# Kernel optimization log

Measured on AMD Instinct MI355X. Metric: run time of the kernel, lower is better.

## Reference

```python
import jax, jax.numpy as jnp
import numpy as np
from jax import lax

PATCH_SIZE = 7
NEIGH_SIZE = 9
SIGMA = 2.0
EPS = 1e-05


def _gaussian_kernel(sigma, sz):
    mid = sz // 2
    ax = np.arange(sz) - mid
    g = np.exp(-(ax[:, None] ** 2 + ax[None, :] ** 2) / (2.0 * sigma ** 2)) / (2.0 * np.pi * sigma ** 2)
    return g.astype(np.float32)


KERNEL = jnp.asarray(_gaussian_kernel(SIGMA, PATCH_SIZE))[None, None]  # (1,1,7,7)

_half = NEIGH_SIZE // 2
SHIFTS = jnp.asarray(
    [(x, y) for x in range(-_half, NEIGH_SIZE - _half)
     for y in range(-_half, NEIGH_SIZE - _half) if (x, y) != (0, 0)],
    dtype=jnp.int32)  # (80, 2) — xshift outer loop, yshift inner, matching torch order
SHIFTS4 = jnp.asarray([(-1, 0), (1, 0), (0, -1), (0, 1)], dtype=jnp.int32)


def _translate(img, tx, ty):
    # Faithful to torch affine_grid + grid_sample(nearest, zeros, align_corners=False):
    # a 'translation' of tx in normalized coords samples input at pixel j + tx*W/2.
    # H, W even and tx, ty integers -> exact integer pixel shifts, zero padding.
    H, W = img.shape
    px = jnp.arange(W) + tx * (W // 2)
    py = jnp.arange(H) + ty * (H // 2)
    mask = ((py >= 0) & (py < H))[:, None] & ((px >= 0) & (px < W))[None, :]
    out = img[jnp.clip(py, 0, H - 1)[:, None], jnp.clip(px, 0, W - 1)[None, :]]
    return jnp.where(mask, out, jnp.zeros((), img.dtype))


def _blur(x):
    # x: (N, H, W); conv2d with gaussian kernel, stride 1, padding 3 (same for 7x7)
    y = lax.conv_general_dilated(x[:, None], KERNEL, (1, 1), [(3, 3), (3, 3)],
                                 dimension_numbers=('NCHW', 'OIHW', 'NCHW'))
    return y[:, 0]


def _dp_batch(img2d, shifts):
    # Dp for a batch of shifts: shift, diff, square, gaussian blur
    shifted = jax.vmap(lambda s: _translate(img2d, s[0], s[1]))(shifts)  # (N,H,W)
    return _blur((img2d[None] - shifted) ** 2)


def setup_inputs() -> dict:
    key = jax.random.key(0)
    k1, k2 = jax.random.split(key)
    image1 = jax.random.normal(k1, (1, 1, 1024, 1024), dtype=jnp.float32)
    image2 = jax.random.normal(k2, (1, 1, 1024, 1024), dtype=jnp.float32)
    return {"image1": image1, "image2": image2}


def reference(image1, image2):
    img1 = image1[0, 0]  # (H, W)
    img2 = image2[0, 0]
    H, W = img1.shape
    reduce_size = (PATCH_SIZE + NEIGH_SIZE - 2) // 2  # = 7
    # Vimg: average of 4 single-pixel-neighborhood Dp's on image1, + eps
    Vimg = _dp_batch(img1, SHIFTS4).sum(axis=0) / 4.0 + EPS  # (H, W)
    # 80-shift MIND responses on image2
    D2 = _dp_batch(img2, SHIFTS)  # (80, H, W)
    mind = jnp.exp(-D2 / Vimg[None])
    # torch slices: dim1 end index is (C - reduce_size) = 1-7 = -6 -> H-6;
    # dim2 end index is (H - reduce_size). Replicated exactly (H == W).
    out = mind[:, reduce_size:H + 1 - reduce_size, reduce_size:H - reduce_size]
    mx = jnp.max(out, axis=0)
    return jnp.mean(out / mx[None])
```

## Files before the change

kernel.cpp:

```cpp
#include <hip/hip_runtime.h>
#include <cmath>

#define IMG_W 1024
#define TW 64
#define TH 16
#define PW 70
#define PH 22

struct GK { float gh[7]; float gv[7]; };

__global__ __launch_bounds__(256)
void mind_fused(const float* __restrict__ img1, const float* __restrict__ img2,
                float* __restrict__ out, GK gk)
{
    __shared__ float s1[4][PH][PW];
    __shared__ float s2[6][PH][TW];

    const int tx = (int)threadIdx.x;
    const int ty = (int)threadIdx.y;
    const int x0 = 7 + (int)blockIdx.x * TW;
    const int y0 = 7 + (int)blockIdx.y * TH;

    #pragma unroll
    for (int k = 0; k < 6; ++k) {
        const int r = 4 * k + ty;
        if (r < PH) {
            const int yy = min(y0 - 3 + r, 1023);
            const int yp = yy ^ 512;
            const float* __restrict__ r2  = img2 + yy * IMG_W;
            const float* __restrict__ r2p = img2 + yp * IMG_W;
            const float* __restrict__ r1  = img1 + yy * IMG_W;
            const float* __restrict__ r1p = img1 + yp * IMG_W;
            #pragma unroll
            for (int h = 0; h < 2; ++h) {
                const int c = tx + 64 * h;
                if (h == 0 || tx < PW - 64) {
                    const int xx = min(x0 - 3 + c, 1023);
                    const int xp = xx ^ 512;
                    const float a = r2[xx], b = r2[xp], cc = r2p[xx], d = r2p[xp];
                    const float a2 = a * a;
                    const float tb = a - b, tc = a - cc, td = a - d;
                    s1[0][r][c] = fmaf(tb, tb, -a2);
                    s1[1][r][c] = fmaf(tc, tc, -a2);
                    s1[2][r][c] = fmaf(td, td, -a2);
                    const float u = r1[xx], ub = r1[xp], uc = r1p[xx];
                    const float su = u - ub, sv = u - uc;
                    s1[3][r][c] = fmaf(u, u + u, fmaf(su, su, sv * sv));
                }
            }
        }
    }
    __syncthreads();

    #pragma unroll
    for (int k = 0; k < 6; ++k) {
        const int r = 4 * k + ty;
        if (r < PH) {
            float hlo = 0, hhi = 0, hv = 0, dlo = 0, dhi = 0, hu = 0;
            #pragma unroll
            for (int kx = 0; kx < 7; ++kx) {
                const float g = gk.gh[kx];
                const bool lo = (((x0 - 3 + tx + kx) & 512) == 0);
                const float gl  = lo ? g : 0.f;
                const float gh_ = lo ? 0.f : g;
                const float Hv = s1[0][r][tx + kx];
                const float Vv = s1[1][r][tx + kx];
                const float Dv = s1[2][r][tx + kx];
                const float Uv = s1[3][r][tx + kx];
                hlo = fmaf(gl,  Hv, hlo);
                hhi = fmaf(gh_, Hv, hhi);
                hv  = fmaf(g,   Vv, hv);
                dlo = fmaf(gl,  Dv, dlo);
                dhi = fmaf(gh_, Dv, dhi);
                hu  = fmaf(g,   Uv, hu);
            }
            s2[0][r][tx] = hlo; s2[1][r][tx] = hhi; s2[2][r][tx] = hv;
            s2[3][r][tx] = dlo; s2[4][r][tx] = dhi; s2[5][r][tx] = hu;
        }
    }
    __syncthreads();

    float f0[10], f1[10], f2[10], f3[10], f4[10], f5[10];
    #pragma unroll
    for (int r = 0; r < 10; ++r) {
        const int rr = 4 * ty + r;
        f0[r] = s2[0][rr][tx]; f1[r] = s2[1][rr][tx]; f2[r] = s2[2][rr][tx];
        f3[r] = s2[3][rr][tx]; f4[r] = s2[4][rr][tx]; f5[r] = s2[5][rr][tx];
    }

    const int xo = x0 + tx;
    float tsum = 0.f;
    #pragma unroll
    for (int k = 0; k < 4; ++k) {
        const int i  = 4 * ty + k;
        const int yo = y0 + i;
        float Ph = 0, Qh = 0, Pv = 0, Qv = 0, Ppp = 0, Pmp = 0, Ppm = 0, Pmm = 0, V4 = 0;
        #pragma unroll
        for (int ky = 0; ky < 7; ++ky) {
            const float g = gk.gv[ky];
            const bool ylo = (((yo - 3 + ky) & 512) == 0);
            const float wl = ylo ? g : 0.f;
            const float wh = ylo ? 0.f : g;
            const int idx = k + ky;
            Ph  = fmaf(g,  f0[idx], Ph);
            Qh  = fmaf(g,  f1[idx], Qh);
            Pv  = fmaf(wl, f2[idx], Pv);
            Qv  = fmaf(wh, f2[idx], Qv);
            Ppp = fmaf(wl, f3[idx], Ppp);
            Ppm = fmaf(wh, f3[idx], Ppm);
            Pmp = fmaf(wl, f4[idx], Pmp);
            Pmm = fmaf(wh, f4[idx], Pmm);
            V4  = fmaf(g,  f5[idx], V4);
        }
        const float V = fmaf(V4, 0.25f, 1e-5f);
        const float invV = 1.0f / V;
        float M = fminf(0.f, Ph);
        M = fminf(M, Qh);  M = fminf(M, Pv);  M = fminf(M, Qv);
        M = fminf(M, Ppp); M = fminf(M, Pmp); M = fminf(M, Ppm); M = fminf(M, Pmm);
        const float pix = 72.f * __expf(M * invV)
            + __expf((M - Ph ) * invV) + __expf((M - Qh ) * invV)
            + __expf((M - Pv ) * invV) + __expf((M - Qv ) * invV)
            + __expf((M - Ppp) * invV) + __expf((M - Pmp) * invV)
            + __expf((M - Ppm) * invV) + __expf((M - Pmm) * invV);
        const bool active = (xo <= 1016) && (yo <= 1017);
        tsum += active ? pix : 0.f;
    }

    #pragma unroll
    for (int off = 32; off > 0; off >>= 1)
        tsum += __shfl_down(tsum, off, 64);
    __shared__ float wsum[4];
    if (tx == 0) wsum[ty] = tsum;
    __syncthreads();
    if (tx == 0 && ty == 0) {
        const float bt = wsum[0] + wsum[1] + wsum[2] + wsum[3];
        atomicAdd(out, bt * (1.0f / 81688800.0f));
    }
}

extern "C" void kernel_launch(void* const* d_in, const int* in_sizes, int n_in,
                              void* d_out, int out_size, void* d_ws, size_t ws_size,
                              hipStream_t stream) {
    const float* img1 = (const float*)d_in[0];
    const float* img2 = (const float*)d_in[1];
    float* out = (float*)d_out;

    GK gk;
    for (int i = 0; i < 7; ++i) {
        const double d = i - 3;
        gk.gh[i] = (float)std::exp(-(d * d) / 8.0);
        gk.gv[i] = (float)(std::exp(-(d * d) / 8.0) / (8.0 * M_PI));
    }

    hipMemsetAsync(d_out, 0, sizeof(float), stream);
    dim3 block(64, 4);
    dim3 grid(16, 64);
    mind_fused<<<grid, block, 0, stream>>>(img1, img2, out, gk);
}
```

Baseline: 80.76 us.

## Restructure fused MIND kernel into row-sweep with register sliding window

Replaces the 2D tile with 64x4 threads and two shared-memory stages with 128-thread blocks. Each block sweeps down 18 rows, computing the horizontal blur through a double-buffered float4 shared row and keeping a 7-row sliding window of horizontal results in registers for the vertical blur. This removes the large shared-memory staging arrays and the re-reading of vertical halos. In exchange it adds a block barrier on every row step, recomputes horizontal halo columns in each block (6 of 128 threads idle), and uses smaller blocks, which leaves less parallelism per block.

```diff
diff --git a/kernel.cpp b/kernel.cpp
--- a/kernel.cpp
+++ b/kernel.cpp
@@ -2,140 +2,125 @@
 #include <cmath>
 
 #define IMG_W 1024
-#define TW 64
-#define TH 16
-#define PW 70
-#define PH 22
+#define NT    128
+#define OC    (NT - 6)
+#define ROWS  12
+#define STEPS (ROWS + 6)
+#define PADW  (NT + 6)
 
 struct GK { float gh[7]; float gv[7]; };
 
-__global__ __launch_bounds__(256)
-void mind_fused(const float* __restrict__ img1, const float* __restrict__ img2,
+__global__ __launch_bounds__(NT)
+void mind_sweep(const float* __restrict__ img1, const float* __restrict__ img2,
                 float* __restrict__ out, GK gk)
 {
-    __shared__ float s1[4][PH][PW];
-    __shared__ float s2[6][PH][TW];
+    __shared__ float4 buf[2][PADW];
 
     const int tx = (int)threadIdx.x;
-    const int ty = (int)threadIdx.y;
-    const int x0 = 7 + (int)blockIdx.x * TW;
-    const int y0 = 7 + (int)blockIdx.y * TH;
+    const int X0 = 7 + (int)blockIdx.x * OC;
+    const int Y0 = 7 + (int)blockIdx.y * ROWS;
+
+    const int sx_raw = X0 - 3 + tx;
+    const int sx  = min(sx_raw, 1023);
+    const int sxp = sx ^ 512;
+    const bool xok = (tx >= 3) && (tx <= NT - 4) && (sx_raw <= 1016);
+
+    float glx[7], ghx[7];
+    #pragma unroll
+    for (int kx = 0; kx < 7; ++kx) {
+        const bool lo = (((sx_raw + kx - 3) & 512) == 0);
+        glx[kx] = lo ? gk.gh[kx] : 0.f;
+        ghx[kx] = lo ? 0.f : gk.gh[kx];
+    }
+
+    float wHlo[7] = {0}, wHhi[7] = {0}, wV[7] = {0},
+          wDlo[7] = {0}, wDhi[7] = {0}, wU[7] = {0};
+    float tsum = 0.f;
 
     #pragma unroll
-    for (int k = 0; k < 6; ++k) {
-        const int r = 4 * k + ty;
-        if (r < PH) {
-            const int yy = min(y0 - 3 + r, 1023);
-            const int yp = yy ^ 512;
-            const float* __restrict__ r2  = img2 + yy * IMG_W;
-            const float* __restrict__ r2p = img2 + yp * IMG_W;
-            const float* __restrict__ r1  = img1 + yy * IMG_W;
-            const float* __restrict__ r1p = img1 + yp * IMG_W;
-            #pragma unroll
-            for (int h = 0; h < 2; ++h) {
-                const int c = tx + 64 * h;
-                if (h == 0 || tx < PW - 64) {
-                    const int xx = min(x0 - 3 + c, 1023);
-                    const int xp = xx ^ 512;
-                    const float a = r2[xx], b = r2[xp], cc = r2p[xx], d = r2p[xp];
-                    const float a2 = a * a;
-                    const float tb = a - b, tc = a - cc, td = a - d;
-                    s1[0][r][c] = fmaf(tb, tb, -a2);
-                    s1[1][r][c] = fmaf(tc, tc, -a2);
-                    s1[2][r][c] = fmaf(td, td, -a2);
-                    const float u = r1[xx], ub = r1[xp], uc = r1p[xx];
-                    const float su = u - ub, sv = u - uc;
-                    s1[3][r][c] = fmaf(u, u + u, fmaf(su, su, sv * sv));
+    for (int s = 0; s < STEPS; ++s) {
+        const int sr  = min(Y0 - 3 + s, 1023);
+        const int srp = sr ^ 512;
+        const float* __restrict__ r2  = img2 + sr  * IMG_W;
+        const float* __restrict__ r2p = img2 + srp * IMG_W;
+        const float* __restrict__ r1  = img1 + sr  * IMG_W;
+        const float* __restrict__ r1p = img1 + srp * IMG_W;
+        const float a  = r2[sx], b = r2[sxp], c = r2p[sx], d = r2p[sxp];
+        const float u  = r1[sx], ub = r1[sxp], uc = r1p[sx];
+        const float a2 = a * a;
+        const float tb = a - b, tc = a - c, td = a - d;
+        const float su = u - ub, sv = u - uc;
+        float4 f;
+        f.x = fmaf(tb, tb, -a2);
+        f.y = fmaf(tc, tc, -a2);
+        f.z = fmaf(td, td, -a2);
+        f.w = fmaf(u, u + u, fmaf(su, su, sv * sv));
+        buf[s & 1][tx + 3] = f;
+        __syncthreads();
+
+        float hHlo = 0, hHhi = 0, hV = 0, hDlo = 0, hDhi = 0, hU = 0;
+        #pragma unroll
+        for (int kx = 0; kx < 7; ++kx) {
+            const float4 g = buf[s & 1][tx + kx];
+            hHlo = fmaf(glx[kx],  g.x, hHlo);
+            hHhi = fmaf(ghx[kx],  g.x, hHhi);
+            hV   = fmaf(gk.gh[kx], g.y, hV);
+            hDlo = fmaf(glx[kx],  g.z, hDlo);
+            hDhi = fmaf(ghx[kx],  g.z, hDhi);
+            hU   = fmaf(gk.gh[kx], g.w, hU);
+        }
+        #pragma unroll
+        for (int i = 0; i < 6; ++i) {
+            wHlo[i] = wHlo[i+1]; wHhi[i] = wHhi[i+1]; wV[i] = wV[i+1];
+            wDlo[i] = wDlo[i+1]; wDhi[i] = wDhi[i+1]; wU[i] = wU[i+1];
+        }
+        wHlo[6] = hHlo; wHhi[6] = hHhi; wV[6] = hV;
+        wDlo[6] = hDlo; wDhi[6] = hDhi; wU[6] = hU;
+
+        if (s >= 6) {
+            const int y = Y0 + s - 6;
+            if (y <= 1017) {
+                float Ph=0,Qh=0,Pv=0,Qv=0,Ppp=0,Ppm=0,Pmp=0,Pmm=0,V4=0;
+                #pragma unroll
+                for (int ky = 0; ky < 7; ++ky) {
+                    const float g = gk.gv[ky];
+                    const bool ylo = (((y - 3 + ky) & 512) == 0);
+                    const float wl = ylo ? g : 0.f;
+                    const float wh = ylo ? 0.f : g;
+                    Ph  = fmaf(g,  wHlo[ky], Ph);
+                    Qh  = fmaf(g,  wHhi[ky], Qh);
+                    Pv  = fmaf(wl, wV[ky],   Pv);
+                    Qv  = fmaf(wh, wV[ky],   Qv);
+                    Ppp = fmaf(wl, wDlo[ky], Ppp);
+                    Ppm = fmaf(wh, wDlo[ky], Ppm);
+                    Pmp = fmaf(wl, wDhi[ky], Pmp);
+                    Pmm = fmaf(wh, wDhi[ky], Pmm);
+                    V4  = fmaf(g,  wU[ky],   V4);
                 }
+                const float V = fmaf(V4, 0.25f, 1e-5f);
+                const float invV = 1.0f / V;
+                float M = fminf(0.f, Ph);
+                M = fminf(M, Qh);  M = fminf(M, Pv);  M = fminf(M, Qv);
+                M = fminf(M, Ppp); M = fminf(M, Pmp); M = fminf(M, Ppm); M = fminf(M, Pmm);
+                const float pix = 72.f * __expf(M * invV)
+                    + __expf((M - Ph ) * invV) + __expf((M - Qh ) * invV)
+                    + __expf((M - Pv ) * invV) + __expf((M - Qv ) * invV)
+                    + __expf((M - Ppp) * invV) + __expf((M - Pmp) * invV)
+                    + __expf((M - Ppm) * invV) + __expf((M - Pmm) * invV);
+                tsum += xok ? pix : 0.f;
             }
         }
-    }
-    __syncthreads();
-
-    #pragma unroll
-    for (int k = 0; k < 6; ++k) {
-        const int r = 4 * k + ty;
-        if (r < PH) {
-            float hlo = 0, hhi = 0, hv = 0, dlo = 0, dhi = 0, hu = 0;
-            #pragma unroll
-            for (int kx = 0; kx < 7; ++kx) {
-                const float g = gk.gh[kx];
-                const bool lo = (((x0 - 3 + tx + kx) & 512) == 0);
-                const float gl  = lo ? g : 0.f;
-                const float gh_ = lo ? 0.f : g;
-                const float Hv = s1[0][r][tx + kx];
-                const float Vv = s1[1][r][tx + kx];
-                const float Dv = s1[2][r][tx + kx];
-                const float Uv = s1[3][r][tx + kx];
-                hlo = fmaf(gl,  Hv, hlo);
-                hhi = fmaf(gh_, Hv, hhi);
-                hv  = fmaf(g,   Vv, hv);
-                dlo = fmaf(gl,  Dv, dlo);
-                dhi = fmaf(gh_, Dv, dhi);
-                hu  = fmaf(g,   Uv, hu);
-            }
-            s2[0][r][tx] = hlo; s2[1][r][tx] = hhi; s2[2][r][tx] = hv;
-            s2[3][r][tx] = dlo; s2[4][r][tx] = dhi; s2[5][r][tx] = hu;
-        }
-    }
-    __syncthreads();
-
-    float f0[10], f1[10], f2[10], f3[10], f4[10], f5[10];
-    #pragma unroll
-    for (int r = 0; r < 10; ++r) {
-        const int rr = 4 * ty + r;
-        f0[r] = s2[0][rr][tx]; f1[r] = s2[1][rr][tx]; f2[r] = s2[2][rr][tx];
-        f3[r] = s2[3][rr][tx]; f4[r] = s2[4][rr][tx]; f5[r] = s2[5][rr][tx];
-    }
-
-    const int xo = x0 + tx;
-    float tsum = 0.f;
-    #pragma unroll
-    for (int k = 0; k < 4; ++k) {
-        const int i  = 4 * ty + k;
-        const int yo = y0 + i;
-        float Ph = 0, Qh = 0, Pv = 0, Qv = 0, Ppp = 0, Pmp = 0, Ppm = 0, Pmm = 0, V4 = 0;
-        #pragma unroll
-        for (int ky = 0; ky < 7; ++ky) {
-            const float g = gk.gv[ky];
-            const bool ylo = (((yo - 3 + ky) & 512) == 0);
-            const float wl = ylo ? g : 0.f;
-            const float wh = ylo ? 0.f : g;
-            const int idx = k + ky;
-            Ph  = fmaf(g,  f0[idx], Ph);
-            Qh  = fmaf(g,  f1[idx], Qh);
-            Pv  = fmaf(wl, f2[idx], Pv);
-            Qv  = fmaf(wh, f2[idx], Qv);
-            Ppp = fmaf(wl, f3[idx], Ppp);
-            Ppm = fmaf(wh, f3[idx], Ppm);
-            Pmp = fmaf(wl, f4[idx], Pmp);
-            Pmm = fmaf(wh, f4[idx], Pmm);
-            V4  = fmaf(g,  f5[idx], V4);
-        }
-        const float V = fmaf(V4, 0.25f, 1e-5f);
-        const float invV = 1.0f / V;
-        float M = fminf(0.f, Ph);
-        M = fminf(M, Qh);  M = fminf(M, Pv);  M = fminf(M, Qv);
-        M = fminf(M, Ppp); M = fminf(M, Pmp); M = fminf(M, Ppm); M = fminf(M, Pmm);
-        const float pix = 72.f * __expf(M * invV)
-            + __expf((M - Ph ) * invV) + __expf((M - Qh ) * invV)
-            + __expf((M - Pv ) * invV) + __expf((M - Qv ) * invV)
-            + __expf((M - Ppp) * invV) + __expf((M - Pmp) * invV)
-            + __expf((M - Ppm) * invV) + __expf((M - Pmm) * invV);
-        const bool active = (xo <= 1016) && (yo <= 1017);
-        tsum += active ? pix : 0.f;
     }
 
     #pragma unroll
     for (int off = 32; off > 0; off >>= 1)
         tsum += __shfl_down(tsum, off, 64);
-    __shared__ float wsum[4];
-    if (tx == 0) wsum[ty] = tsum;
+    __shared__ float wsum[2];
     __syncthreads();
-    if (tx == 0 && ty == 0) {
-        const float bt = wsum[0] + wsum[1] + wsum[2] + wsum[3];
-        atomicAdd(out, bt * (1.0f / 81688800.0f));
-    }
+    if ((tx & 63) == 0) wsum[tx >> 6] = tsum;
+    __syncthreads();
+    if (tx == 0)
+        atomicAdd(out, (wsum[0] + wsum[1]) * (1.0f / 81688800.0f));
 }
 
 extern "C" void kernel_launch(void* const* d_in, const int* in_sizes, int n_in,
@@ -153,7 +138,7 @@
     }
 
     hipMemsetAsync(d_out, 0, sizeof(float), stream);
-    dim3 block(64, 4);
-    dim3 grid(16, 64);
-    mind_fused<<<grid, block, 0, stream>>>(img1, img2, out, gk);
+    dim3 block(NT, 1);
+    dim3 grid(9, 85);
+    mind_sweep<<<grid, block, 0, stream>>>(img1, img2, out, gk);
 }
```

New measurement: 83.98 us. +4.0%, slower.
